# Performance work log

Hardware: AMD Instinct MI355X
Metric: run time of the kernel (lower is better)

Reference implementation:

```python
import jax, jax.numpy as jnp
import numpy as np

PRIOR_VAR = 0.01
NUM_HEADS = 12
EMBED_DIM = 768


def kl_regularizer(mu, logvar):
    kl_loss = (jnp.log(PRIOR_VAR) - 1.0 - logvar
               + jax.nn.softplus(logvar) / PRIOR_VAR
               + jnp.square(mu) / PRIOR_VAR)
    return 0.5 * jnp.mean(kl_loss)


def linear_vdp(mu_in, Sigma_in, w_mu, w_sigma):
    # mu_in, Sigma_in: [..., Din]; w_mu: [Din, Dout]; w_sigma: [Dout]
    mu_out = mu_in @ w_mu
    kl = kl_regularizer(w_mu, w_sigma)
    W_Sigma = jax.nn.softplus(w_sigma)                      # [Dout]
    din = w_mu.shape[0]
    # w_t_Sigma_i_w: w scaled by sqrt(Din)
    w_scaled = w_mu / jnp.sqrt(jnp.float32(din))
    Sigma_1 = Sigma_in @ (w_scaled * w_scaled)              # [..., Dout]
    # x_Sigma_w_x_T: x scaled by Din
    x = mu_in / jnp.float32(din)
    xx_t = jnp.sum(x * x, axis=-1, keepdims=True)
    Sigma_2 = xx_t * W_Sigma
    # tr_Sigma_w_Sigma_in
    Sigma_3 = jnp.sum(Sigma_in, axis=-1, keepdims=True) * W_Sigma / jnp.float32(w_mu.shape[-1])
    Sigma_out = jax.nn.softplus(Sigma_1 + Sigma_2 + Sigma_3)
    return mu_out, Sigma_out, kl


def split_heads(x, B, H, d):
    # [B, S, E] -> [B, H, S, d]
    return x.reshape(B, -1, H, d).transpose(0, 2, 1, 3)


def vdp_attention(mu_q, sg_q, mu_k, sg_k, mu_v, sg_v):
    d = jnp.float32(mu_k.shape[-1])
    sq = jnp.sqrt(d)
    mu_score = jnp.einsum('bhqd,bhkd->bhqk', mu_q, mu_k)
    a = jnp.einsum('bhqd,bhkd->bhqk', mu_q * mu_q / d, sg_k)
    b = jnp.einsum('bhid,bhjd->bhij', mu_k * mu_k / d, sg_q)  # TF matmul(key.., query.., transpose_b)
    c = jnp.einsum('bhqd,bhkd->bhqk', sg_q / sq, sg_k / sq)
    sigma_score = a + b + c
    mu_weights = jax.nn.softmax(mu_score / sq, axis=-1)
    wdim = jnp.float32(mu_weights.shape[-1])
    grad = jnp.square(mu_weights - mu_weights * mu_weights)
    Sigma_weights = grad * (sigma_score / d) / wdim
    mu_out = jnp.einsum('bhqk,bhkd->bhqd', mu_weights, mu_v)
    dterm = jnp.einsum('bhqk,bhkd->bhqd', mu_weights * mu_weights / wdim, sg_v)
    eterm = jnp.einsum('bhqk,bhkd->bhqd', Sigma_weights, mu_v * mu_v / wdim)
    fterm = jnp.einsum('bhqk,bhkd->bhqd', Sigma_weights / jnp.sqrt(wdim), sg_v / jnp.sqrt(wdim))
    out_sigma = jax.nn.softplus(dterm + eterm + fterm)
    return mu_out, out_sigma


def forward(mu_inputs, sigma_inputs, wq_mu, wq_sigma, wk_mu, wk_sigma,
            wv_mu, wv_sigma, wo_mu, wo_sigma):
    B = mu_inputs.shape[0]
    H = NUM_HEADS
    d = EMBED_DIM // H
    # VDP_Dropout with Training=False is identity
    mu_q, sg_q, kl_q = linear_vdp(mu_inputs, sigma_inputs, wq_mu, wq_sigma)
    mu_k, sg_k, kl_k = linear_vdp(mu_inputs, sigma_inputs, wk_mu, wk_sigma)
    mu_v, sg_v, kl_v = linear_vdp(mu_inputs, sigma_inputs, wv_mu, wv_sigma)
    mu_q, sg_q = split_heads(mu_q, B, H, d), split_heads(sg_q, B, H, d)
    mu_k, sg_k = split_heads(mu_k, B, H, d), split_heads(sg_k, B, H, d)
    mu_v, sg_v = split_heads(mu_v, B, H, d), split_heads(sg_v, B, H, d)
    mu_att, sg_att = vdp_attention(mu_q, sg_q, mu_k, sg_k, mu_v, sg_v)
    mu_cat = mu_att.transpose(0, 2, 1, 3).reshape(B, -1, EMBED_DIM)
    sg_cat = sg_att.transpose(0, 2, 1, 3).reshape(B, -1, EMBED_DIM)
    mu_out, Sigma_out, kl_c = linear_vdp(mu_cat, sg_cat, wo_mu, wo_sigma)
    Sigma_out = jax.nn.softplus(Sigma_out)
    kl = kl_q + kl_k + kl_v + kl_c
    return mu_out, Sigma_out, kl


def setup_inputs() -> dict:
    key = jax.random.key(0)
    ks = jax.random.split(key, 12)
    B, S, E = 4, 1024, EMBED_DIM
    glorot_std = np.sqrt(2.0 / (E + E)).astype(np.float32)
    def wsig(k):
        return jax.random.uniform(k, (E,), jnp.float32, -4.6, -2.25)
    return {
        'mu_inputs': jax.random.normal(ks[0], (B, S, E), jnp.float32),
        'sigma_inputs': jax.random.uniform(ks[1], (B, S, E), jnp.float32),
        'wq_mu': jax.random.normal(ks[2], (E, E), jnp.float32) * glorot_std,
        'wq_sigma': wsig(ks[3]),
        'wk_mu': jax.random.normal(ks[4], (E, E), jnp.float32) * glorot_std,
        'wk_sigma': wsig(ks[5]),
        'wv_mu': jax.random.normal(ks[6], (E, E), jnp.float32) * glorot_std,
        'wv_sigma': wsig(ks[7]),
        'wo_mu': jax.random.normal(ks[8], (E, E), jnp.float32) * glorot_std,
        'wo_sigma': wsig(ks[9]),
    }


def reference(mu_inputs, sigma_inputs, wq_mu, wq_sigma, wk_mu, wk_sigma,
              wv_mu, wv_sigma, wo_mu, wo_sigma):
    return forward(mu_inputs, sigma_inputs, wq_mu, wq_sigma, wk_mu, wk_sigma,
                   wv_mu, wv_sigma, wo_mu, wo_sigma)
```

## Files before the change

kernel.cpp:

```cpp
#include <hip/hip_runtime.h>
#include <math.h>

#define E 768
#define NTOK 4096

typedef __attribute__((ext_vector_type(8))) __bf16 bf16x8;
typedef __attribute__((ext_vector_type(4))) float f32x4;
typedef unsigned int u32;
typedef unsigned short u16;
typedef __attribute__((ext_vector_type(4))) u32 u32x4;

#define BFN ((size_t)NTOK * E)
#define WFN ((size_t)E * E)
#define QSC 1.4901161193847656e-08f
#define C2E 0.18033688011112042f

__device__ __forceinline__ float sp_f(float x) {
    return fmaxf(x, 0.f) + log1pf(__expf(-fabsf(x)));
}
__device__ __forceinline__ u16 f2bf(float f) {
    u32 u = __float_as_uint(f);
    u += 0x7fffu + ((u >> 16) & 1u);
    return (u16)(u >> 16);
}
__device__ __forceinline__ u32 pk2(float a, float b) {
    return (u32)f2bf(a) | ((u32)f2bf(b) << 16);
}
__device__ __forceinline__ u32 cvtpk(float a, float b) {
    u32 r; asm("v_cvt_pk_bf16_f32 %0, %1, %2" : "=v"(r) : "v"(a), "v"(b)); return r;
}
__device__ __forceinline__ float ex2(float x) {
    float r; asm("v_exp_f32 %0, %1" : "=v"(r) : "v"(x)); return r;
}
__device__ __forceinline__ float lg2(float x) {
    float r; asm("v_log_f32 %0, %1" : "=v"(r) : "v"(x)); return r;
}
__device__ __forceinline__ float bfl(u32 u) { return __uint_as_float(u << 16); }
__device__ __forceinline__ float bfh(u32 u) { return __uint_as_float(u & 0xffff0000u); }

#define GLL16(gp, lp) __builtin_amdgcn_global_load_lds( \
    (const __attribute__((address_space(1))) u32*)(gp), \
    (__attribute__((address_space(3))) u32*)(lp), 16, 0, 0)

#define SBAR() do { __builtin_amdgcn_sched_barrier(0); \
                    __builtin_amdgcn_s_barrier(); \
                    __builtin_amdgcn_sched_barrier(0); } while (0)
#define VMCNT(N) do { asm volatile("s_waitcnt vmcnt(" #N ")" ::: "memory"); \
                      __builtin_amdgcn_sched_barrier(0); } while (0)

__global__ __launch_bounds__(256) void prep_all(
    const float* __restrict__ mu_in, const float* __restrict__ sg_in,
    const float* __restrict__ wq, const float* __restrict__ wk,
    const float* __restrict__ wvp, const float* __restrict__ wo,
    const float* __restrict__ wqs, const float* __restrict__ wks,
    const float* __restrict__ wvs, const float* __restrict__ wos,
    u16* __restrict__ Xmu, u16* __restrict__ Xsg,
    float* __restrict__ rmu2, float* __restrict__ rsg,
    u16* __restrict__ WtAll, u16* __restrict__ W2tAll,
    float* __restrict__ spws, float* __restrict__ kl_out)
{
    __shared__ float T[32][33];
    __shared__ float r1[4], r2[4];
    const int b = blockIdx.x, tid = threadIdx.x;

    if (b < 2048) {
        const int half = tid >> 7;
        const int n = b * 2 + half;
        const int t2 = tid & 127;
        float s1 = 0.f, s2 = 0.f;
        if (t2 < 96) {
            size_t o = (size_t)n * E + t2 * 8;
            float4 a0 = *(const float4*)(mu_in + o), a1 = *(const float4*)(mu_in + o + 4);
            float4 b0 = *(const float4*)(sg_in + o), b1 = *(const float4*)(sg_in + o + 4);
            *(uint4*)(Xmu + o) = make_uint4(pk2(a0.x, a0.y), pk2(a0.z, a0.w), pk2(a1.x, a1.y), pk2(a1.z, a1.w));
            *(uint4*)(Xsg + o) = make_uint4(pk2(b0.x, b0.y), pk2(b0.z, b0.w), pk2(b1.x, b1.y), pk2(b1.z, b1.w));
            s1 = a0.x*a0.x + a0.y*a0.y + a0.z*a0.z + a0.w*a0.w + a1.x*a1.x + a1.y*a1.y + a1.z*a1.z + a1.w*a1.w;
            s2 = b0.x + b0.y + b0.z + b0.w + b1.x + b1.y + b1.z + b1.w;
        }
        for (int off = 32; off; off >>= 1) {
            s1 += __shfl_xor(s1, off);
            s2 += __shfl_xor(s2, off);
        }
        if ((tid & 63) == 0) { r1[tid >> 6] = s1; r2[tid >> 6] = s2; }
        __syncthreads();
        if (t2 == 0) {
            rmu2[n] = r1[half * 2] + r1[half * 2 + 1];
            rsg[n]  = r2[half * 2] + r2[half * 2 + 1];
        }
    } else if (b < 4352) {
        const int b2 = b - 2048;
        const int z = b2 / 576, rem = b2 - z * 576;
        const float* W = (z == 0) ? wq : (z == 1) ? wk : (z == 2) ? wvp : wo;
        u16* Wt  = WtAll  + (size_t)z * WFN;
        u16* W2t = W2tAll + (size_t)z * WFN;
        const int j0 = (rem % 24) * 32, k0 = (rem / 24) * 32;
        const int r = tid >> 3, c = (tid & 7) * 4;
        float4 v = *(const float4*)(W + (size_t)(k0 + r) * E + j0 + c);
        T[r][c] = v.x; T[r][c + 1] = v.y; T[r][c + 2] = v.z; T[r][c + 3] = v.w;
        __syncthreads();
        const int j = tid >> 3, kc = (tid & 7) * 4;
        float w0 = T[kc][j], w1 = T[kc + 1][j], w2 = T[kc + 2][j], w3 = T[kc + 3][j];
        size_t o = (size_t)(j0 + j) * E + k0 + kc;
        *(uint2*)(Wt + o) = make_uint2(pk2(w0, w1), pk2(w2, w3));
        const float s = 1.f / 768.f;
        *(uint2*)(W2t + o) = make_uint2(pk2(w0 * w0 * s, w1 * w1 * s), pk2(w2 * w2 * s, w3 * w3 * s));
    } else if (b < 4864) {
        const int gid = (b - 4352) * 256 + tid;
        const int gsz = 512 * 256;
        float acc = 0.f;
        const float cw = 100.f / ((float)E * (float)E);
#pragma unroll
        for (int mm = 0; mm < 4; ++mm) {
            const float* w  = (mm == 0) ? wq  : (mm == 1) ? wk  : (mm == 2) ? wvp : wo;
            const float* sv = (mm == 0) ? wqs : (mm == 1) ? wks : (mm == 2) ? wvs : wos;
            for (int i = gid; i < E * E; i += gsz) { float x = w[i]; acc += x * x * cw; }
            for (int i = gid; i < E; i += gsz) { float x = sv[i]; acc += (-x + sp_f(x) * 100.f) * (1.f / (float)E); }
        }
        if (b == 4352 && tid == 0) acc += 4.f * (logf(0.01f) - 1.f);
        for (int off = 32; off; off >>= 1) acc += __shfl_xor(acc, off);
        if ((tid & 63) == 0) r1[tid >> 6] = acc;
        __syncthreads();
        if (tid == 0) atomicAdd(kl_out, 0.5f * (r1[0] + r1[1] + r1[2] + r1[3]));
    } else {
        for (int i = tid; i < 4 * E; i += 256) {
            const float* src;
            int j;
            if (i < E)            { src = wqs; j = i; }
            else if (i < 2 * E)   { src = wks; j = i - E; }
            else if (i < 3 * E)   { src = wvs; j = i - 2 * E; }
            else                  { src = wos; j = i - 3 * E; }
            spws[i] = sp_f(src[j]);
        }
    }
}

__global__ __launch_bounds__(128) void rowstats_bf16_kernel(
    const u16* __restrict__ mu, const u16* __restrict__ sg,
    float* __restrict__ rmu2, float* __restrict__ rsg)
{
    const int n = blockIdx.x, tid = threadIdx.x;
    float s1 = 0.f, s2 = 0.f;
    if (tid < 96) {
        uint4 um = *(const uint4*)(mu + (size_t)n * E + tid * 8);
        uint4 us = *(const uint4*)(sg + (size_t)n * E + tid * 8);
        u32 ua[4] = {um.x, um.y, um.z, um.w};
        u32 ub[4] = {us.x, us.y, us.z, us.w};
#pragma unroll
        for (int j = 0; j < 4; ++j) {
            float a0 = bfl(ua[j]), a1 = bfh(ua[j]);
            s1 += a0 * a0 + a1 * a1;
            s2 += bfl(ub[j]) + bfh(ub[j]);
        }
    }
    for (int off = 32; off; off >>= 1) {
        s1 += __shfl_xor(s1, off);
        s2 += __shfl_xor(s2, off);
    }
    __shared__ float r1[2], r2[2];
    if ((tid & 63) == 0) { r1[tid >> 6] = s1; r2[tid >> 6] = s2; }
    __syncthreads();
    if (tid == 0) { rmu2[n] = r1[0] + r1[1]; rsg[n] = r2[0] + r2[1]; }
}

template<int MODE>
__global__ __launch_bounds__(256, 3) void linear_fused(
    const u16* __restrict__ Am, const u16* __restrict__ As,
    const u16* __restrict__ Wt, const u16* __restrict__ W2t,
    const float* __restrict__ spws, const float* __restrict__ rmu2, const float* __restrict__ rsg,
    float* __restrict__ mu_out, float* __restrict__ sg_out, u16* __restrict__ QKVB)
{
    __shared__ __align__(16) u16 L[24576];

    const int wgid = blockIdx.x;
    const int xcd = wgid & 7, local = wgid >> 3;
    const int m_blk = xcd * 4 + (local & 3);
    const int n_blk = local >> 2;
    const int m0 = m_blk * 128, col0 = n_blk * 64;
    const int tid = threadIdx.x, wv = tid >> 6, lane = tid & 63;
    const int g = lane >> 4, q15 = lane & 15;

    const u16* sp_[6];
    {
        const int rA = tid >> 2, cA = tid & 3;
        const int rB = 64 + rA;
        const int csA = (cA ^ ((rA >> 1) & 3)) << 3;
        const int csB = (cA ^ ((rB >> 1) & 3)) << 3;
        sp_[0] = Am  + (size_t)(m0 + rA) * E + csA;
        sp_[1] = Am  + (size_t)(m0 + rB) * E + csB;
        sp_[2] = As  + (size_t)(m0 + rA) * E + csA;
        sp_[3] = As  + (size_t)(m0 + rB) * E + csB;
        sp_[4] = Wt  + (size_t)(col0 + rA) * E + csA;
        sp_[5] = W2t + (size_t)(col0 + rA) * E + csA;
    }

    f32x4 acc1[2][4], acc2[2][4];
#pragma unroll
    for (int mt = 0; mt < 2; ++mt)
#pragma unroll
        for (int nt = 0; nt < 4; ++nt) {
            acc1[mt][nt] = (f32x4){0.f, 0.f, 0.f, 0.f};
            acc2[mt][nt] = (f32x4){0.f, 0.f, 0.f, 0.f};
        }

#pragma unroll
    for (int j = 0; j < 6; ++j)
        GLL16(sp_[j], &L[j * 2048 + tid * 8]);

    for (int t = 0; t < 24; ++t) {
        SBAR();
        const int tn = (t < 23) ? t + 1 : 23;
        const int nb = ((t & 1) ^ 1) * 12288;
#pragma unroll
        for (int j = 0; j < 6; ++j)
            GLL16(sp_[j] + tn * 32, &L[nb + j * 2048 + tid * 8]);
        VMCNT(6);
        SBAR();
        const int cb = (t & 1) * 12288;
        bf16x8 am[2], asg[2];
#pragma unroll
        for (int mt = 0; mt < 2; ++mt) {
            int r = wv * 32 + mt * 16 + q15;
            int c = (g ^ ((r >> 1) & 3)) << 3;
            am[mt]  = *(const bf16x8*)&L[cb + r * 32 + c];
            asg[mt] = *(const bf16x8*)&L[cb + 4096 + r * 32 + c];
        }
        __builtin_amdgcn_s_setprio(1);
#pragma unroll
        for (int nt = 0; nt < 4; ++nt) {
            int rb = nt * 16 + q15;
            int c = (g ^ ((rb >> 1) & 3)) << 3;
            bf16x8 bw = *(const bf16x8*)&L[cb + 8192 + rb * 32 + c];
            bf16x8 b2 = *(const bf16x8*)&L[cb + 10240 + rb * 32 + c];
            acc1[0][nt] = __builtin_amdgcn_mfma_f32_16x16x32_bf16(am[0], bw, acc1[0][nt], 0, 0, 0);
            acc1[1][nt] = __builtin_amdgcn_mfma_f32_16x16x32_bf16(am[1], bw, acc1[1][nt], 0, 0, 0);
            acc2[0][nt] = __builtin_amdgcn_mfma_f32_16x16x32_bf16(asg[0], b2, acc2[0][nt], 0, 0, 0);
            acc2[1][nt] = __builtin_amdgcn_mfma_f32_16x16x32_bf16(asg[1], b2, acc2[1][nt], 0, 0, 0);
        }
        __builtin_amdgcn_s_setprio(0);
    }
    __syncthreads();

    const float inv2 = 1.f / (768.f * 768.f), invd = 1.f / 768.f;
    float rr[2][4];
#pragma unroll
    for (int mt = 0; mt < 2; ++mt)
#pragma unroll
        for (int r = 0; r < 4; ++r) {
            int row = m0 + wv * 32 + mt * 16 + g * 4 + r;
            rr[mt][r] = rmu2[row] * inv2 + rsg[row] * invd;
        }

    if (MODE == 0) {
#pragma unroll
        for (int mt = 0; mt < 2; ++mt)
#pragma unroll
            for (int nt = 0; nt < 4; ++nt)
#pragma unroll
                for (int r = 0; r < 4; ++r) {
                    int row = m0 + wv * 32 + mt * 16 + g * 4 + r;
                    int col = col0 + nt * 16 + q15;
                    float mu = acc1[mt][nt][r];
                    float sg = sp_f(sp_f(acc2[mt][nt][r] + rr[mt][r] * spws[col]));
                    mu_out[(size_t)row * E + col] = mu;
                    sg_out[(size_t)row * E + col] = sg;
                }
    } else {
        const int proj = n_blk / 12, h = n_blk % 12;
        float sgv[2][4][4];
#pragma unroll
        for (int mt = 0; mt < 2; ++mt)
#pragma unroll
            for (int nt = 0; nt < 4; ++nt)
#pragma unroll
                for (int r = 0; r < 4; ++r) {
                    int col = col0 + nt * 16 + q15;
                    sgv[mt][nt][r] = sp_f(acc2[mt][nt][r] + rr[mt][r] * spws[col]);
                }
        const int bb = m0 >> 10;
        if (proj < 2) {
            const int s0 = (m0 & 1023);
            const int sl = tid >> 1, hh = tid & 1;
            size_t gbase = ((size_t)(bb * 12 + h) << 16) + ((size_t)(s0 + sl) << 6) + hh * 32;
#pragma unroll
            for (int a = 0; a < 3; ++a) {
                __syncthreads();
#pragma unroll
                for (int mt = 0; mt < 2; ++mt)
#pragma unroll
                    for (int nt = 0; nt < 4; ++nt)
#pragma unroll
                        for (int r = 0; r < 4; ++r) {
                            float mu = acc1[mt][nt][r], sg = sgv[mt][nt][r];
                            float v = (a == 0) ? mu : (a == 1) ? sg :
                                      (proj == 0 ? (mu * mu + sg) * QSC : mu * mu * QSC);
                            L[(wv * 32 + mt * 16 + g * 4 + r) * 72 + nt * 16 + q15] = f2bf(v);
                        }
                __syncthreads();
                u16* dst = QKVB + (size_t)(proj * 3 + a) * BFN;
#pragma unroll
                for (int j = 0; j < 4; ++j)
                    *(uint4*)(dst + gbase + j * 8) = *(const uint4*)&L[sl * 72 + hh * 32 + j * 8];
            }
        } else {
            const int s0 = m0 & 1023;
#pragma unroll
            for (int a = 0; a < 3; ++a) {
                __syncthreads();
#pragma unroll
                for (int mt = 0; mt < 2; ++mt)
#pragma unroll
                    for (int nt = 0; nt < 4; ++nt)
#pragma unroll
                        for (int r = 0; r < 4; ++r) {
                            float mu = acc1[mt][nt][r], sg = sgv[mt][nt][r];
                            float v = (a == 0) ? mu : (a == 1) ? sg * 0.0009765625f : mu * mu + sg;
                            L[(nt * 16 + q15) * 136 + wv * 32 + g * 8 + mt * 4 + r] = f2bf(v);
                        }
                __syncthreads();
                const int d = tid >> 2, sc = (tid & 3) * 32;
                u16* dst = QKVB + (size_t)(6 + a) * BFN;
                size_t ga = ((size_t)((bb * 12 + h) * 64 + d) << 10) + s0 + sc;
                *(uint4*)(dst + ga)      = *(const uint4*)&L[d * 136 + sc];
                *(uint4*)(dst + ga + 8)  = *(const uint4*)&L[d * 136 + sc + 8];
                *(uint4*)(dst + ga + 16) = *(const uint4*)&L[d * 136 + sc + 16];
                *(uint4*)(dst + ga + 24) = *(const uint4*)&L[d * 136 + sc + 24];
            }
        }
    }
}

#define KB0 0
#define KB1 6144
#define VB0 12288
#define VB1 18432
__global__ __launch_bounds__(256, 3) void vdp_attn8(
    const u16* __restrict__ Kmu, const u16* __restrict__ Ksg, const u16* __restrict__ Asq,
    const u16* __restrict__ Qmu, const u16* __restrict__ Q1v, const u16* __restrict__ Q2v,
    const u16* __restrict__ Vmu, const u16* __restrict__ Vsg, const u16* __restrict__ Vw2,
    u16* __restrict__ om, u16* __restrict__ osg)
{
    __shared__ __align__(16) u16 L[24576];

    const int wgid = blockIdx.x;
    const int seq = (wgid & 7) * 96 + (wgid >> 3);
    const int bh = seq >> 4, qt = seq & 15;
    const int tid = threadIdx.x, wv = tid >> 6, lane = tid & 63;
    const int g = lane >> 4, q15 = lane & 15;
    const size_t hb = (size_t)bh << 16;

    const size_t qoff = hb + (size_t)((qt * 64 + wv * 16 + q15) << 6) + g * 8;
    bf16x8 bq0 = *(const bf16x8*)(Qmu + qoff), bq1 = *(const bf16x8*)(Qmu + qoff + 32);
    bf16x8 b10 = *(const bf16x8*)(Q1v + qoff), b11 = *(const bf16x8*)(Q1v + qoff + 32);
    bf16x8 b20 = *(const bf16x8*)(Q2v + qoff), b21 = *(const bf16x8*)(Q2v + qoff + 32);

    const int sr = tid >> 3, sc8 = tid & 7;
    const size_t koffA = hb + (size_t)sr * 64 + ((sc8 ^ (sr & 7)) << 3);
    const size_t koffB = hb + (size_t)(sr + 32) * 64 + ((sc8 ^ (sr & 7)) << 3);
    const int vr = tid >> 2, vc = tid & 3;
    const size_t voff = hb + (size_t)vr * 1024 + ((vc ^ ((vr >> 1) & 3)) << 3);

    float m2 = -3.0e38f;
    float lacc[4] = {0.f, 0.f, 0.f, 0.f};
    GLL16(Kmu + koffA, &L[0 + wv * 512]);
    GLL16(Kmu + koffB, &L[2048 + wv * 512]);
    __syncthreads();
    for (int t = 0; t < 16; ++t) {
        SBAR();
        const int tn = (t < 15) ? t + 1 : 15;
        const int nb = (t & 1) ? 0 : 4096;
        GLL16(Kmu + koffA + ((size_t)tn << 12), &L[nb + wv * 512]);
        GLL16(Kmu + koffB + ((size_t)tn << 12), &L[nb + 2048 + wv * 512]);
        VMCNT(2);
        SBAR();
        const int kb = (t & 1) ? 4096 : 0;
        f32x4 sc[4];
#pragma unroll
        for (int kt = 0; kt < 4; ++kt) sc[kt] = (f32x4){0.f, 0.f, 0.f, 0.f};
        __builtin_amdgcn_s_setprio(1);
#pragma unroll
        for (int kt = 0; kt < 4; ++kt) {
            int row = kt * 16 + q15, ra = kb + (row << 6);
            bf16x8 k0 = *(const bf16x8*)&L[ra + ((g ^ (row & 7)) << 3)];
            bf16x8 k1 = *(const bf16x8*)&L[ra + (((g + 4) ^ (row & 7)) << 3)];
            sc[kt] = __builtin_amdgcn_mfma_f32_16x16x32_bf16(k0, bq0, sc[kt], 0, 0, 0);
            sc[kt] = __builtin_amdgcn_mfma_f32_16x16x32_bf16(k1, bq1, sc[kt], 0, 0, 0);
        }
        __builtin_amdgcn_s_setprio(0);
        float t0 = fmaxf(fmaxf(sc[0][0], sc[0][1]), fmaxf(sc[0][2], sc[0][3]));
        float t1 = fmaxf(fmaxf(sc[1][0], sc[1][1]), fmaxf(sc[1][2], sc[1][3]));
        float t2 = fmaxf(fmaxf(sc[2][0], sc[2][1]), fmaxf(sc[2][2], sc[2][3]));
        float t3 = fmaxf(fmaxf(sc[3][0], sc[3][1]), fmaxf(sc[3][2], sc[3][3]));
        float tm = fmaxf(fmaxf(t0, t1), fmaxf(t2, t3)) * C2E;
        if (tm > m2 + 8.f) {
            float f = ex2(m2 - tm);
            lacc[0] *= f; lacc[1] *= f; lacc[2] *= f; lacc[3] *= f;
            m2 = tm;
        }
#pragma unroll
        for (int kt = 0; kt < 4; ++kt)
#pragma unroll
            for (int r = 0; r < 4; ++r)
                lacc[kt] += ex2(fmaf(sc[kt][r], C2E, -m2));
    }
    __syncthreads();
    float l = (lacc[0] + lacc[1]) + (lacc[2] + lacc[3]);
#pragma unroll
    for (int off = 16; off <= 32; off <<= 1) {
        float mo = __shfl_xor(m2, off), lo = __shfl_xor(l, off);
        float nm = fmaxf(m2, mo);
        l = l * ex2(m2 - nm) + lo * ex2(mo - nm);
        m2 = nm;
    }
    const float M = m2 + lg2(l);

    f32x4 accm[4], accd[4], acce[4];
#pragma unroll
    for (int nt = 0; nt < 4; ++nt) {
        accm[nt] = (f32x4){0.f, 0.f, 0.f, 0.f};
        accd[nt] = (f32x4){0.f, 0.f, 0.f, 0.f};
        acce[nt] = (f32x4){0.f, 0.f, 0.f, 0.f};
    }

    GLL16(Kmu + koffA, &L[KB0 + 0    + wv * 512]);
    GLL16(Ksg + koffA, &L[KB0 + 2048 + wv * 512]);
    GLL16(Asq + koffA, &L[KB0 + 4096 + wv * 512]);
    GLL16(Vmu + voff, &L[VB0 + 0    + wv * 512]);
    GLL16(Vsg + voff, &L[VB0 + 2048 + wv * 512]);
    GLL16(Vw2 + voff, &L[VB0 + 4096 + wv * 512]);
    __syncthreads();

    for (int t = 0; t < 32; ++t) {
        SBAR();
        const int tn = (t < 31) ? t + 1 : 31;
        const size_t ka = (size_t)tn << 11;
        const size_t va = (size_t)tn << 5;
        const int nbK = (t & 1) ? KB0 : KB1;
        const int nbV = (t & 1) ? VB0 : VB1;
        GLL16(Kmu + koffA + ka, &L[nbK + 0    + wv * 512]);
        GLL16(Ksg + koffA + ka, &L[nbK + 2048 + wv * 512]);
        GLL16(Asq + koffA + ka, &L[nbK + 4096 + wv * 512]);
        GLL16(Vmu + voff + va,  &L[nbV + 0    + wv * 512]);
        GLL16(Vsg + voff + va,  &L[nbV + 2048 + wv * 512]);
        GLL16(Vw2 + voff + va,  &L[nbV + 4096 + wv * 512]);
        VMCNT(6);
        SBAR();

        const int kb = (t & 1) ? KB1 : KB0;
        const int vb = (t & 1) ? VB1 : VB0;
        f32x4 sc[2], sgc[2];
#pragma unroll
        for (int kt = 0; kt < 2; ++kt) { sc[kt] = (f32x4){0.f,0.f,0.f,0.f}; sgc[kt] = (f32x4){0.f,0.f,0.f,0.f}; }
        __builtin_amdgcn_s_setprio(1);
#pragma unroll
        for (int kt = 0; kt < 2; ++kt) {
            int row = kt * 16 + q15, ra = kb + (row << 6);
            int ca = ((g ^ (row & 7)) << 3), cb = (((g + 4) ^ (row & 7)) << 3);
            sc[kt]  = __builtin_amdgcn_mfma_f32_16x16x32_bf16(*(const bf16x8*)&L[ra + ca],        bq0, sc[kt],  0, 0, 0);
            sc[kt]  = __builtin_amdgcn_mfma_f32_16x16x32_bf16(*(const bf16x8*)&L[ra + cb],        bq1, sc[kt],  0, 0, 0);
            sgc[kt] = __builtin_amdgcn_mfma_f32_16x16x32_bf16(*(const bf16x8*)&L[2048 + ra + ca], b10, sgc[kt], 0, 0, 0);
            sgc[kt] = __builtin_amdgcn_mfma_f32_16x16x32_bf16(*(const bf16x8*)&L[2048 + ra + cb], b11, sgc[kt], 0, 0, 0);
            sgc[kt] = __builtin_amdgcn_mfma_f32_16x16x32_bf16(*(const bf16x8*)&L[4096 + ra + ca], b20, sgc[kt], 0, 0, 0);
            sgc[kt] = __builtin_amdgcn_mfma_f32_16x16x32_bf16(*(const bf16x8*)&L[4096 + ra + cb], b21, sgc[kt], 0, 0, 0);
        }
        __builtin_amdgcn_s_setprio(0);

        float p[8], p2v[8], swv[8];
#pragma unroll
        for (int kt = 0; kt < 2; ++kt)
#pragma unroll
            for (int r = 0; r < 4; ++r) {
                int j = kt * 4 + r;
                float pv = ex2(fmaf(sc[kt][r], C2E, -M));
                float pp = pv * pv;
                float gq = pv - pp;
                p[j] = pv; p2v[j] = pp; swv[j] = gq * gq * sgc[kt][r];
            }
        u32x4 ua  = {cvtpk(p[0], p[1]),     cvtpk(p[2], p[3]),     cvtpk(p[4], p[5]),     cvtpk(p[6], p[7])};
        u32x4 ubv = {cvtpk(p2v[0], p2v[1]), cvtpk(p2v[2], p2v[3]), cvtpk(p2v[4], p2v[5]), cvtpk(p2v[6], p2v[7])};
        u32x4 ucv = {cvtpk(swv[0], swv[1]), cvtpk(swv[2], swv[3]), cvtpk(swv[4], swv[5]), cvtpk(swv[6], swv[7])};
        bf16x8 pa  = *(const bf16x8*)&ua;
        bf16x8 p2a = *(const bf16x8*)&ubv;
        bf16x8 swa = *(const bf16x8*)&ucv;

        __builtin_amdgcn_s_setprio(1);
#pragma unroll
        for (int nt = 0; nt < 4; ++nt) {
            int row = nt * 16 + q15;
            int vi = vb + (row << 5) + ((g ^ ((q15 >> 1) & 3)) << 3);
            accm[nt] = __builtin_amdgcn_mfma_f32_16x16x32_bf16(pa,  *(const bf16x8*)&L[vi],        accm[nt], 0, 0, 0);
            accd[nt] = __builtin_amdgcn_mfma_f32_16x16x32_bf16(p2a, *(const bf16x8*)&L[vi + 2048], accd[nt], 0, 0, 0);
            acce[nt] = __builtin_amdgcn_mfma_f32_16x16x32_bf16(swa, *(const bf16x8*)&L[vi + 4096], acce[nt], 0, 0, 0);
        }
        __builtin_amdgcn_s_setprio(0);
    }

    const int b_ = bh / 12, h_ = bh % 12;
#pragma unroll
    for (int nt = 0; nt < 4; ++nt)
#pragma unroll
        for (int r = 0; r < 4; ++r) {
            int srow = qt * 64 + wv * 16 + g * 4 + r;
            int d = nt * 16 + q15;
            size_t o = (size_t)(b_ * 1024 + srow) * E + h_ * 64 + d;
            om[o]  = f2bf(accm[nt][r]);
            osg[o] = f2bf(sp_f(accd[nt][r] + acce[nt][r]));
        }
}

extern "C" void kernel_launch(void* const* d_in, const int* in_sizes, int n_in,
                              void* d_out, int out_size, void* d_ws, size_t ws_size,
                              hipStream_t stream)
{
    const float* mu_in = (const float*)d_in[0];
    const float* sg_in = (const float*)d_in[1];
    const float* wq  = (const float*)d_in[2];
    const float* wqs = (const float*)d_in[3];
    const float* wk  = (const float*)d_in[4];
    const float* wks = (const float*)d_in[5];
    const float* wvp = (const float*)d_in[6];
    const float* wvs = (const float*)d_in[7];
    const float* wo  = (const float*)d_in[8];
    const float* wos = (const float*)d_in[9];

    float* out_mu = (float*)d_out;
    float* out_sg = out_mu + (size_t)NTOK * E;
    float* kl_out = out_mu + 2 * (size_t)NTOK * E;

    float* ws = (float*)d_ws;
    size_t off = 0;
    auto allocf = [&](size_t n) { float* p = ws + off; off += n; return p; };
    float* rmu2  = allocf(NTOK);
    float* rsgs  = allocf(NTOK);
    float* armu2 = allocf(NTOK);
    float* arsg  = allocf(NTOK);
    float* spws  = allocf(4 * E);

    u16* ub = (u16*)(ws + off);
    size_t uoff = 0;
    auto allocu = [&](size_t n) { u16* p = ub + uoff; uoff += n; return p; };
    u16* Xmu    = allocu(BFN);
    u16* Xsg    = allocu(BFN);
    u16* WtAll  = allocu(4 * WFN);
    u16* W2tAll = allocu(4 * WFN);
    u16* QKVB   = allocu(9 * BFN);
    u16* amu_b  = allocu(BFN);
    u16* asg_b  = allocu(BFN);
    (void)ws_size; (void)in_sizes; (void)n_in; (void)out_size;

    hipMemsetAsync(kl_out, 0, 4, stream);
    prep_all<<<4865, 256, 0, stream>>>(mu_in, sg_in, wq, wk, wvp, wo,
                                       wqs, wks, wvs, wos,
                                       Xmu, Xsg, rmu2, rsgs, WtAll, W2tAll,
                                       spws, kl_out);

    linear_fused<1><<<1152, 256, 0, stream>>>(Xmu, Xsg, WtAll, W2tAll, spws, rmu2, rsgs,
                                              nullptr, nullptr, QKVB);

    vdp_attn8<<<768, 256, 0, stream>>>(QKVB + 3 * BFN, QKVB + 4 * BFN, QKVB + 1 * BFN,
                                       QKVB + 0 * BFN, QKVB + 2 * BFN, QKVB + 5 * BFN,
                                       QKVB + 6 * BFN, QKVB + 7 * BFN, QKVB + 8 * BFN,
                                       amu_b, asg_b);

    rowstats_bf16_kernel<<<NTOK, 128, 0, stream>>>(amu_b, asg_b, armu2, arsg);
    linear_fused<0><<<384, 256, 0, stream>>>(amu_b, asg_b, WtAll + 3 * WFN, W2tAll + 3 * WFN,
                                             spws + 3 * E, armu2, arsg,
                                             out_mu, out_sg, nullptr);
}
```

Measured before the change: 223.3 us.

## Use 512-thread 128x128 tiles for fused QKV projection kernel

Splits the templated linear kernel into a dedicated QKV kernel with 512 threads and 128x128 output tiles (8 waves in a 4x2 grid) and a separate output-projection kernel. Wider tiles halve the number of workgroups and let each loaded A tile be reused across twice as many output columns, cutting global/LDS traffic for the activations. The epilogue is reworked so each tile spans two heads. This uses more LDS (64KB double buffer) and lowers occupancy per CU.

```diff
diff --git a/kernel.cpp b/kernel.cpp
--- a/kernel.cpp
+++ b/kernel.cpp
@@ -162,12 +162,156 @@
     if (tid == 0) { rmu2[n] = r1[0] + r1[1]; rsg[n] = r2[0] + r2[1]; }
 }
 
-template<int MODE>
-__global__ __launch_bounds__(256, 3) void linear_fused(
+__global__ __launch_bounds__(512, 4) void linear_qkv512(
     const u16* __restrict__ Am, const u16* __restrict__ As,
     const u16* __restrict__ Wt, const u16* __restrict__ W2t,
     const float* __restrict__ spws, const float* __restrict__ rmu2, const float* __restrict__ rsg,
-    float* __restrict__ mu_out, float* __restrict__ sg_out, u16* __restrict__ QKVB)
+    u16* __restrict__ QKVB)
+{
+    __shared__ __align__(16) u16 L[32768];
+
+    const int wgid = blockIdx.x;
+    const int xcd = wgid & 7, local = wgid >> 3;
+    const int m_blk = xcd * 4 + (local & 3);
+    const int n_blk = local >> 2;
+    const int m0 = m_blk * 128, col0 = n_blk * 128;
+    const int tid = threadIdx.x, wv = tid >> 6, lane = tid & 63;
+    const int g = lane >> 4, q15 = lane & 15;
+    const int wr = wv & 3, wc = wv >> 2;
+
+    const u16* sp_[4];
+    {
+        const int r = tid >> 2, c = tid & 3;
+        const int cs = (c ^ ((r >> 1) & 3)) << 3;
+        sp_[0] = Am  + (size_t)(m0 + r) * E + cs;
+        sp_[1] = As  + (size_t)(m0 + r) * E + cs;
+        sp_[2] = Wt  + (size_t)(col0 + r) * E + cs;
+        sp_[3] = W2t + (size_t)(col0 + r) * E + cs;
+    }
+
+    f32x4 acc1[2][4], acc2[2][4];
+#pragma unroll
+    for (int mt = 0; mt < 2; ++mt)
+#pragma unroll
+        for (int nt = 0; nt < 4; ++nt) {
+            acc1[mt][nt] = (f32x4){0.f, 0.f, 0.f, 0.f};
+            acc2[mt][nt] = (f32x4){0.f, 0.f, 0.f, 0.f};
+        }
+
+#pragma unroll
+    for (int j = 0; j < 4; ++j)
+        GLL16(sp_[j], &L[j * 4096 + tid * 8]);
+
+    for (int t = 0; t < 24; ++t) {
+        SBAR();
+        const int tn = (t < 23) ? t + 1 : 23;
+        const int nb = ((t & 1) ^ 1) * 16384;
+#pragma unroll
+        for (int j = 0; j < 4; ++j)
+            GLL16(sp_[j] + tn * 32, &L[nb + j * 4096 + tid * 8]);
+        VMCNT(4);
+        SBAR();
+        const int cb = (t & 1) * 16384;
+        bf16x8 am[2], asg[2];
+#pragma unroll
+        for (int mt = 0; mt < 2; ++mt) {
+            int r = wr * 32 + mt * 16 + q15;
+            int c = (g ^ ((r >> 1) & 3)) << 3;
+            am[mt]  = *(const bf16x8*)&L[cb + r * 32 + c];
+            asg[mt] = *(const bf16x8*)&L[cb + 4096 + r * 32 + c];
+        }
+        __builtin_amdgcn_s_setprio(1);
+#pragma unroll
+        for (int nt = 0; nt < 4; ++nt) {
+            int rb = wc * 64 + nt * 16 + q15;
+            int c = (g ^ ((rb >> 1) & 3)) << 3;
+            bf16x8 bw = *(const bf16x8*)&L[cb + 8192 + rb * 32 + c];
+            bf16x8 b2 = *(const bf16x8*)&L[cb + 12288 + rb * 32 + c];
+            acc1[0][nt] = __builtin_amdgcn_mfma_f32_16x16x32_bf16(am[0], bw, acc1[0][nt], 0, 0, 0);
+            acc1[1][nt] = __builtin_amdgcn_mfma_f32_16x16x32_bf16(am[1], bw, acc1[1][nt], 0, 0, 0);
+            acc2[0][nt] = __builtin_amdgcn_mfma_f32_16x16x32_bf16(asg[0], b2, acc2[0][nt], 0, 0, 0);
+            acc2[1][nt] = __builtin_amdgcn_mfma_f32_16x16x32_bf16(asg[1], b2, acc2[1][nt], 0, 0, 0);
+        }
+        __builtin_amdgcn_s_setprio(0);
+    }
+    __syncthreads();
+
+    const float inv2 = 1.f / (768.f * 768.f), invd = 1.f / 768.f;
+    float rr_[2][4];
+#pragma unroll
+    for (int mt = 0; mt < 2; ++mt)
+#pragma unroll
+        for (int r = 0; r < 4; ++r) {
+            int row = m0 + wr * 32 + mt * 16 + g * 4 + r;
+            rr_[mt][r] = rmu2[row] * inv2 + rsg[row] * invd;
+        }
+    float sgv[2][4][4];
+#pragma unroll
+    for (int mt = 0; mt < 2; ++mt)
+#pragma unroll
+        for (int nt = 0; nt < 4; ++nt)
+#pragma unroll
+            for (int r = 0; r < 4; ++r) {
+                int col = col0 + wc * 64 + nt * 16 + q15;
+                sgv[mt][nt][r] = sp_f(acc2[mt][nt][r] + rr_[mt][r] * spws[col]);
+            }
+
+    const int proj = n_blk / 6, h2 = n_blk % 6;
+    const int bb = m0 >> 10, s0 = m0 & 1023;
+    if (proj < 2) {
+        const int sl = tid >> 2, seg = tid & 3, hh = seg >> 1, hf = seg & 1;
+        size_t gbase = ((size_t)(bb * 12 + 2 * h2 + hh) << 16) + ((size_t)(s0 + sl) << 6) + hf * 32;
+#pragma unroll
+        for (int a = 0; a < 3; ++a) {
+            __syncthreads();
+#pragma unroll
+            for (int mt = 0; mt < 2; ++mt)
+#pragma unroll
+                for (int nt = 0; nt < 4; ++nt)
+#pragma unroll
+                    for (int r = 0; r < 4; ++r) {
+                        float mu = acc1[mt][nt][r], sg = sgv[mt][nt][r];
+                        float v = (a == 0) ? mu : (a == 1) ? sg :
+                                  (proj == 0 ? (mu * mu + sg) * QSC : mu * mu * QSC);
+                        L[(wr * 32 + mt * 16 + g * 4 + r) * 136 + wc * 64 + nt * 16 + q15] = f2bf(v);
+                    }
+            __syncthreads();
+            u16* dst = QKVB + (size_t)(proj * 3 + a) * BFN;
+#pragma unroll
+            for (int j = 0; j < 4; ++j)
+                *(uint4*)(dst + gbase + j * 8) = *(const uint4*)&L[sl * 136 + hh * 64 + hf * 32 + j * 8];
+        }
+    } else {
+        const int dcol = tid >> 2, qq = tid & 3;
+        const int head = dcol >> 6, d = dcol & 63;
+        size_t ga = ((size_t)((bb * 12 + 2 * h2 + head) * 64 + d) << 10) + s0 + qq * 32;
+#pragma unroll
+        for (int a = 0; a < 3; ++a) {
+            __syncthreads();
+#pragma unroll
+            for (int mt = 0; mt < 2; ++mt)
+#pragma unroll
+                for (int nt = 0; nt < 4; ++nt)
+#pragma unroll
+                    for (int r = 0; r < 4; ++r) {
+                        float mu = acc1[mt][nt][r], sg = sgv[mt][nt][r];
+                        float v = (a == 0) ? mu : (a == 1) ? sg * 0.0009765625f : mu * mu + sg;
+                        L[(wc * 64 + nt * 16 + q15) * 136 + wr * 32 + g * 8 + mt * 4 + r] = f2bf(v);
+                    }
+            __syncthreads();
+            u16* dst = QKVB + (size_t)(6 + a) * BFN;
+#pragma unroll
+            for (int j = 0; j < 4; ++j)
+                *(uint4*)(dst + ga + j * 8) = *(const uint4*)&L[dcol * 136 + qq * 32 + j * 8];
+        }
+    }
+}
+
+__global__ __launch_bounds__(256, 3) void linear_oproj(
+    const u16* __restrict__ Am, const u16* __restrict__ As,
+    const u16* __restrict__ Wt, const u16* __restrict__ W2t,
+    const float* __restrict__ spws, const float* __restrict__ rmu2, const float* __restrict__ rsg,
+    float* __restrict__ mu_out, float* __restrict__ sg_out)
 {
     __shared__ __align__(16) u16 L[24576];
 
@@ -241,92 +385,21 @@
     __syncthreads();
 
     const float inv2 = 1.f / (768.f * 768.f), invd = 1.f / 768.f;
-    float rr[2][4];
 #pragma unroll
     for (int mt = 0; mt < 2; ++mt)
 #pragma unroll
         for (int r = 0; r < 4; ++r) {
             int row = m0 + wv * 32 + mt * 16 + g * 4 + r;
-            rr[mt][r] = rmu2[row] * inv2 + rsg[row] * invd;
-        }
-
-    if (MODE == 0) {
-#pragma unroll
-        for (int mt = 0; mt < 2; ++mt)
-#pragma unroll
-            for (int nt = 0; nt < 4; ++nt)
-#pragma unroll
-                for (int r = 0; r < 4; ++r) {
-                    int row = m0 + wv * 32 + mt * 16 + g * 4 + r;
-                    int col = col0 + nt * 16 + q15;
-                    float mu = acc1[mt][nt][r];
-                    float sg = sp_f(sp_f(acc2[mt][nt][r] + rr[mt][r] * spws[col]));
-                    mu_out[(size_t)row * E + col] = mu;
-                    sg_out[(size_t)row * E + col] = sg;
-                }
-    } else {
-        const int proj = n_blk / 12, h = n_blk % 12;
-        float sgv[2][4][4];
-#pragma unroll
-        for (int mt = 0; mt < 2; ++mt)
-#pragma unroll
-            for (int nt = 0; nt < 4; ++nt)
-#pragma unroll
-                for (int r = 0; r < 4; ++r) {
-                    int col = col0 + nt * 16 + q15;
-                    sgv[mt][nt][r] = sp_f(acc2[mt][nt][r] + rr[mt][r] * spws[col]);
-                }
-        const int bb = m0 >> 10;
-        if (proj < 2) {
-            const int s0 = (m0 & 1023);
-            const int sl = tid >> 1, hh = tid & 1;
-            size_t gbase = ((size_t)(bb * 12 + h) << 16) + ((size_t)(s0 + sl) << 6) + hh * 32;
-#pragma unroll
-            for (int a = 0; a < 3; ++a) {
-                __syncthreads();
-#pragma unroll
-                for (int mt = 0; mt < 2; ++mt)
-#pragma unroll
-                    for (int nt = 0; nt < 4; ++nt)
-#pragma unroll
-                        for (int r = 0; r < 4; ++r) {
-                            float mu = acc1[mt][nt][r], sg = sgv[mt][nt][r];
-                            float v = (a == 0) ? mu : (a == 1) ? sg :
-                                      (proj == 0 ? (mu * mu + sg) * QSC : mu * mu * QSC);
-                            L[(wv * 32 + mt * 16 + g * 4 + r) * 72 + nt * 16 + q15] = f2bf(v);
-                        }
-                __syncthreads();
-                u16* dst = QKVB + (size_t)(proj * 3 + a) * BFN;
-#pragma unroll
-                for (int j = 0; j < 4; ++j)
-                    *(uint4*)(dst + gbase + j * 8) = *(const uint4*)&L[sl * 72 + hh * 32 + j * 8];
+            float rr = rmu2[row] * inv2 + rsg[row] * invd;
+#pragma unroll
+            for (int nt = 0; nt < 4; ++nt) {
+                int col = col0 + nt * 16 + q15;
+                float mu = acc1[mt][nt][r];
+                float sg = sp_f(sp_f(acc2[mt][nt][r] + rr * spws[col]));
+                mu_out[(size_t)row * E + col] = mu;
+                sg_out[(size_t)row * E + col] = sg;
             }
-        } else {
-            const int s0 = m0 & 1023;
-#pragma unroll
-            for (int a = 0; a < 3; ++a) {
-                __syncthreads();
-#pragma unroll
-                for (int mt = 0; mt < 2; ++mt)
-#pragma unroll
-                    for (int nt = 0; nt < 4; ++nt)
-#pragma unroll
-                        for (int r = 0; r < 4; ++r) {
-                            float mu = acc1[mt][nt][r], sg = sgv[mt][nt][r];
-                            float v = (a == 0) ? mu : (a == 1) ? sg * 0.0009765625f : mu * mu + sg;
-                            L[(nt * 16 + q15) * 136 + wv * 32 + g * 8 + mt * 4 + r] = f2bf(v);
-                        }
-                __syncthreads();
-                const int d = tid >> 2, sc = (tid & 3) * 32;
-                u16* dst = QKVB + (size_t)(6 + a) * BFN;
-                size_t ga = ((size_t)((bb * 12 + h) * 64 + d) << 10) + s0 + sc;
-                *(uint4*)(dst + ga)      = *(const uint4*)&L[d * 136 + sc];
-                *(uint4*)(dst + ga + 8)  = *(const uint4*)&L[d * 136 + sc + 8];
-                *(uint4*)(dst + ga + 16) = *(const uint4*)&L[d * 136 + sc + 16];
-                *(uint4*)(dst + ga + 24) = *(const uint4*)&L[d * 136 + sc + 24];
-            }
-        }
-    }
+        }
 }
 
 #define KB0 0
@@ -553,8 +626,7 @@
                                        Xmu, Xsg, rmu2, rsgs, WtAll, W2tAll,
                                        spws, kl_out);
 
-    linear_fused<1><<<1152, 256, 0, stream>>>(Xmu, Xsg, WtAll, W2tAll, spws, rmu2, rsgs,
-                                              nullptr, nullptr, QKVB);
+    linear_qkv512<<<576, 512, 0, stream>>>(Xmu, Xsg, WtAll, W2tAll, spws, rmu2, rsgs, QKVB);
 
     vdp_attn8<<<768, 256, 0, stream>>>(QKVB + 3 * BFN, QKVB + 4 * BFN, QKVB + 1 * BFN,
                                        QKVB + 0 * BFN, QKVB + 2 * BFN, QKVB + 5 * BFN,
@@ -562,7 +634,6 @@
                                        amu_b, asg_b);
 
     rowstats_bf16_kernel<<<NTOK, 128, 0, stream>>>(amu_b, asg_b, armu2, arsg);
-    linear_fused<0><<<384, 256, 0, stream>>>(amu_b, asg_b, WtAll + 3 * WFN, W2tAll + 3 * WFN,
-                                             spws + 3 * E, armu2, arsg,
-                                             out_mu, out_sg, nullptr);
-}
+    linear_oproj<<<384, 256, 0, stream>>>(amu_b, asg_b, WtAll + 3 * WFN, W2tAll + 3 * WFN,
+                                          spws + 3 * E, armu2, arsg, out_mu, out_sg);
+}
```

Measured after the change: 229.2 us (median of 2 runs). +2.6%, slower.

## Fuse output row statistics into attention epilogue and widen score-pass key tiles

Applied to the files above, without the earlier changes.

Drops the separate rowstats kernel and accumulates per-row sum of squared mu and sum of sigma in the attention epilogue, via lane shuffles and atomicAdd into zeroed buffers. This removes a kernel launch and a re-read of the bf16 attention outputs. The first softmax-statistics pass now loads 128-key tiles per iteration instead of 64, halving loop iterations and barriers. The trade-off is atomic contention, a memset, and statistics taken from unrounded fp32 rather than bf16 values.

```diff
diff --git a/kernel.cpp b/kernel.cpp
--- a/kernel.cpp
+++ b/kernel.cpp
@@ -134,42 +134,14 @@
     }
 }
 
-__global__ __launch_bounds__(128) void rowstats_bf16_kernel(
-    const u16* __restrict__ mu, const u16* __restrict__ sg,
-    float* __restrict__ rmu2, float* __restrict__ rsg)
-{
-    const int n = blockIdx.x, tid = threadIdx.x;
-    float s1 = 0.f, s2 = 0.f;
-    if (tid < 96) {
-        uint4 um = *(const uint4*)(mu + (size_t)n * E + tid * 8);
-        uint4 us = *(const uint4*)(sg + (size_t)n * E + tid * 8);
-        u32 ua[4] = {um.x, um.y, um.z, um.w};
-        u32 ub[4] = {us.x, us.y, us.z, us.w};
-#pragma unroll
-        for (int j = 0; j < 4; ++j) {
-            float a0 = bfl(ua[j]), a1 = bfh(ua[j]);
-            s1 += a0 * a0 + a1 * a1;
-            s2 += bfl(ub[j]) + bfh(ub[j]);
-        }
-    }
-    for (int off = 32; off; off >>= 1) {
-        s1 += __shfl_xor(s1, off);
-        s2 += __shfl_xor(s2, off);
-    }
-    __shared__ float r1[2], r2[2];
-    if ((tid & 63) == 0) { r1[tid >> 6] = s1; r2[tid >> 6] = s2; }
-    __syncthreads();
-    if (tid == 0) { rmu2[n] = r1[0] + r1[1]; rsg[n] = r2[0] + r2[1]; }
-}
-
-template<int MODE>
+template<int MODE, int NBUF>
 __global__ __launch_bounds__(256, 3) void linear_fused(
     const u16* __restrict__ Am, const u16* __restrict__ As,
     const u16* __restrict__ Wt, const u16* __restrict__ W2t,
     const float* __restrict__ spws, const float* __restrict__ rmu2, const float* __restrict__ rsg,
     float* __restrict__ mu_out, float* __restrict__ sg_out, u16* __restrict__ QKVB)
 {
-    __shared__ __align__(16) u16 L[24576];
+    __shared__ __align__(16) u16 L[NBUF * 12288];
 
     const int wgid = blockIdx.x;
     const int xcd = wgid & 7, local = wgid >> 3;
@@ -333,11 +305,12 @@
 #define KB1 6144
 #define VB0 12288
 #define VB1 18432
-__global__ __launch_bounds__(256, 3) void vdp_attn8(
+__global__ __launch_bounds__(256, 3) void vdp_attn9(
     const u16* __restrict__ Kmu, const u16* __restrict__ Ksg, const u16* __restrict__ Asq,
     const u16* __restrict__ Qmu, const u16* __restrict__ Q1v, const u16* __restrict__ Q2v,
     const u16* __restrict__ Vmu, const u16* __restrict__ Vsg, const u16* __restrict__ Vw2,
-    u16* __restrict__ om, u16* __restrict__ osg)
+    u16* __restrict__ om, u16* __restrict__ osg,
+    float* __restrict__ armu2, float* __restrict__ arsg)
 {
     __shared__ __align__(16) u16 L[24576];
 
@@ -355,30 +328,31 @@
 
     const int sr = tid >> 3, sc8 = tid & 7;
     const size_t koffA = hb + (size_t)sr * 64 + ((sc8 ^ (sr & 7)) << 3);
-    const size_t koffB = hb + (size_t)(sr + 32) * 64 + ((sc8 ^ (sr & 7)) << 3);
     const int vr = tid >> 2, vc = tid & 3;
     const size_t voff = hb + (size_t)vr * 1024 + ((vc ^ ((vr >> 1) & 3)) << 3);
 
     float m2 = -3.0e38f;
     float lacc[4] = {0.f, 0.f, 0.f, 0.f};
-    GLL16(Kmu + koffA, &L[0 + wv * 512]);
-    GLL16(Kmu + koffB, &L[2048 + wv * 512]);
+#pragma unroll
+    for (int s = 0; s < 4; ++s)
+        GLL16(Kmu + koffA + s * 2048, &L[s * 2048 + tid * 8]);
     __syncthreads();
-    for (int t = 0; t < 16; ++t) {
+    for (int t = 0; t < 8; ++t) {
         SBAR();
-        const int tn = (t < 15) ? t + 1 : 15;
-        const int nb = (t & 1) ? 0 : 4096;
-        GLL16(Kmu + koffA + ((size_t)tn << 12), &L[nb + wv * 512]);
-        GLL16(Kmu + koffB + ((size_t)tn << 12), &L[nb + 2048 + wv * 512]);
-        VMCNT(2);
+        const int tn = (t < 7) ? t + 1 : 7;
+        const int nb = (t & 1) ? 0 : 8192;
+#pragma unroll
+        for (int s = 0; s < 4; ++s)
+            GLL16(Kmu + koffA + (size_t)tn * 8192 + s * 2048, &L[nb + s * 2048 + tid * 8]);
+        VMCNT(4);
         SBAR();
-        const int kb = (t & 1) ? 4096 : 0;
-        f32x4 sc[4];
-#pragma unroll
-        for (int kt = 0; kt < 4; ++kt) sc[kt] = (f32x4){0.f, 0.f, 0.f, 0.f};
+        const int kb = (t & 1) ? 8192 : 0;
+        f32x4 sc[8];
+#pragma unroll
+        for (int kt = 0; kt < 8; ++kt) sc[kt] = (f32x4){0.f, 0.f, 0.f, 0.f};
         __builtin_amdgcn_s_setprio(1);
 #pragma unroll
-        for (int kt = 0; kt < 4; ++kt) {
+        for (int kt = 0; kt < 8; ++kt) {
             int row = kt * 16 + q15, ra = kb + (row << 6);
             bf16x8 k0 = *(const bf16x8*)&L[ra + ((g ^ (row & 7)) << 3)];
             bf16x8 k1 = *(const bf16x8*)&L[ra + (((g + 4) ^ (row & 7)) << 3)];
@@ -386,21 +360,22 @@
             sc[kt] = __builtin_amdgcn_mfma_f32_16x16x32_bf16(k1, bq1, sc[kt], 0, 0, 0);
         }
         __builtin_amdgcn_s_setprio(0);
-        float t0 = fmaxf(fmaxf(sc[0][0], sc[0][1]), fmaxf(sc[0][2], sc[0][3]));
-        float t1 = fmaxf(fmaxf(sc[1][0], sc[1][1]), fmaxf(sc[1][2], sc[1][3]));
-        float t2 = fmaxf(fmaxf(sc[2][0], sc[2][1]), fmaxf(sc[2][2], sc[2][3]));
-        float t3 = fmaxf(fmaxf(sc[3][0], sc[3][1]), fmaxf(sc[3][2], sc[3][3]));
-        float tm = fmaxf(fmaxf(t0, t1), fmaxf(t2, t3)) * C2E;
-        if (tm > m2 + 8.f) {
-            float f = ex2(m2 - tm);
+        float tmx = -3.0e38f;
+#pragma unroll
+        for (int kt = 0; kt < 8; ++kt)
+#pragma unroll
+            for (int r = 0; r < 4; ++r) tmx = fmaxf(tmx, sc[kt][r]);
+        tmx *= C2E;
+        if (tmx > m2 + 8.f) {
+            float f = ex2(m2 - tmx);
             lacc[0] *= f; lacc[1] *= f; lacc[2] *= f; lacc[3] *= f;
-            m2 = tm;
-        }
-#pragma unroll
-        for (int kt = 0; kt < 4; ++kt)
+            m2 = tmx;
+        }
+#pragma unroll
+        for (int kt = 0; kt < 8; ++kt)
 #pragma unroll
             for (int r = 0; r < 4; ++r)
-                lacc[kt] += ex2(fmaf(sc[kt][r], C2E, -m2));
+                lacc[kt & 3] += ex2(fmaf(sc[kt][r], C2E, -m2));
     }
     __syncthreads();
     float l = (lacc[0] + lacc[1]) + (lacc[2] + lacc[3]);
@@ -496,15 +471,31 @@
 
     const int b_ = bh / 12, h_ = bh % 12;
 #pragma unroll
-    for (int nt = 0; nt < 4; ++nt)
-#pragma unroll
-        for (int r = 0; r < 4; ++r) {
-            int srow = qt * 64 + wv * 16 + g * 4 + r;
+    for (int r = 0; r < 4; ++r) {
+        int srow = qt * 64 + wv * 16 + g * 4 + r;
+        int n = b_ * 1024 + srow;
+        float s1 = 0.f, s2 = 0.f;
+#pragma unroll
+        for (int nt = 0; nt < 4; ++nt) {
             int d = nt * 16 + q15;
-            size_t o = (size_t)(b_ * 1024 + srow) * E + h_ * 64 + d;
-            om[o]  = f2bf(accm[nt][r]);
-            osg[o] = f2bf(sp_f(accd[nt][r] + acce[nt][r]));
-        }
+            float mu = accm[nt][r];
+            float sg = sp_f(accd[nt][r] + acce[nt][r]);
+            size_t o = (size_t)n * E + h_ * 64 + d;
+            om[o]  = f2bf(mu);
+            osg[o] = f2bf(sg);
+            s1 += mu * mu;
+            s2 += sg;
+        }
+#pragma unroll
+        for (int off = 1; off < 16; off <<= 1) {
+            s1 += __shfl_xor(s1, off);
+            s2 += __shfl_xor(s2, off);
+        }
+        if (q15 == 0) {
+            atomicAdd(&armu2[n], s1);
+            atomicAdd(&arsg[n], s2);
+        }
+    }
 }
 
 extern "C" void kernel_launch(void* const* d_in, const int* in_sizes, int n_in,
@@ -548,21 +539,21 @@
     (void)ws_size; (void)in_sizes; (void)n_in; (void)out_size;
 
     hipMemsetAsync(kl_out, 0, 4, stream);
+    hipMemsetAsync(armu2, 0, 2 * NTOK * sizeof(float), stream);
     prep_all<<<4865, 256, 0, stream>>>(mu_in, sg_in, wq, wk, wvp, wo,
                                        wqs, wks, wvs, wos,
                                        Xmu, Xsg, rmu2, rsgs, WtAll, W2tAll,
                                        spws, kl_out);
 
-    linear_fused<1><<<1152, 256, 0, stream>>>(Xmu, Xsg, WtAll, W2tAll, spws, rmu2, rsgs,
-                                              nullptr, nullptr, QKVB);
-
-    vdp_attn8<<<768, 256, 0, stream>>>(QKVB + 3 * BFN, QKVB + 4 * BFN, QKVB + 1 * BFN,
+    linear_fused<1, 2><<<1152, 256, 0, stream>>>(Xmu, Xsg, WtAll, W2tAll, spws, rmu2, rsgs,
+                                                 nullptr, nullptr, QKVB);
+
+    vdp_attn9<<<768, 256, 0, stream>>>(QKVB + 3 * BFN, QKVB + 4 * BFN, QKVB + 1 * BFN,
                                        QKVB + 0 * BFN, QKVB + 2 * BFN, QKVB + 5 * BFN,
                                        QKVB + 6 * BFN, QKVB + 7 * BFN, QKVB + 8 * BFN,
-                                       amu_b, asg_b);
-
-    rowstats_bf16_kernel<<<NTOK, 128, 0, stream>>>(amu_b, asg_b, armu2, arsg);
-    linear_fused<0><<<384, 256, 0, stream>>>(amu_b, asg_b, WtAll + 3 * WFN, W2tAll + 3 * WFN,
-                                             spws + 3 * E, armu2, arsg,
-                                             out_mu, out_sg, nullptr);
-}
+                                       amu_b, asg_b, armu2, arsg);
+
+    linear_fused<0, 2><<<384, 256, 0, stream>>>(amu_b, asg_b, WtAll + 3 * WFN, W2tAll + 3 * WFN,
+                                                spws + 3 * E, armu2, arsg,
+                                                out_mu, out_sg, nullptr);
+}
```

Result: no change. 222.2 us (median of 2 runs) (-0.5%).
